# Optimization experiments

Hardware: AMD Instinct MI355X
Metric: run time of the kernel (lower is better)

## Reference

```python
import jax, jax.numpy as jnp
import numpy as np

BS, N, K, D = 8, 2048, 32, 64
H_MOD, H_STATE, H_MSG = 128, 128, 128
NB, BSZ, NG, BPG = 4, 8, 1, 4  # dendritic tree: K = NB*BSZ, NB = NG*BPG
MOD_IN = K + 2 * D + 1   # 161
MOD_OUT = K + 1 + D      # 97
STATE_IN = 2 * D + 1     # 129
MSG_IN = 2 * D           # 128


def setup_inputs() -> dict:
    key = jax.random.key(0)
    ks = jax.random.split(key, 16)

    def w(k, shape, fan_sum):
        return jax.random.normal(k, shape, jnp.float32) * (2.0 / fan_sum) ** 0.5

    inp = {
        'h': jax.random.normal(ks[0], (BS, N, D), jnp.float32) * 0.1,
        'prev_messages': jax.random.normal(ks[1], (BS, N, D), jnp.float32) * 0.1,
        'hebbian_traces': jax.random.uniform(ks[2], (BS, N, K), jnp.float32),
        'decay_logit': jax.random.normal(ks[3], (BS, N), jnp.float32),
        'primitives': jax.random.normal(ks[4], (BS, N, D), jnp.float32) * 0.1,
        'mod_w1': w(ks[5], (N, H_MOD, MOD_IN), MOD_IN + H_MOD),
        'mod_b1': jnp.zeros((N, H_MOD), jnp.float32),
        'mod_w2': w(ks[6], (N, H_MOD, MOD_OUT), H_MOD + MOD_OUT),
        'mod_b2': jnp.zeros((N, MOD_OUT), jnp.float32),
        'state_w1': w(ks[7], (N, H_STATE, STATE_IN), STATE_IN + H_STATE),
        'state_b1': jnp.zeros((N, H_STATE), jnp.float32),
        'state_w2': w(ks[8], (N, H_STATE, D), H_STATE + D),
        'state_b2': jnp.zeros((N, D), jnp.float32),
        'msg_w1': w(ks[9], (N, H_MSG, MSG_IN), MSG_IN + H_MSG),
        'msg_b1': jnp.zeros((N, H_MSG), jnp.float32),
        'msg_w2': w(ks[10], (N, H_MSG, D), H_MSG + D),
        'msg_b2': jnp.zeros((N, D), jnp.float32),
        'dendrite_branch_w': jnp.full((N, NB, BSZ, D), 1.0 / BSZ, jnp.float32),
        'dendrite_group_w': jnp.full((N, NG, BPG, D), 1.0 / BPG, jnp.float32),
        'conn_indices': jnp.sort(jax.random.randint(ks[11], (N, K), 0, N), axis=-1),
    }
    return inp


def reference(h, prev_messages, hebbian_traces, decay_logit, primitives,
              mod_w1, mod_b1, mod_w2, mod_b2,
              state_w1, state_b1, state_w2, state_b2,
              msg_w1, msg_b1, msg_w2, msg_b2,
              dendrite_branch_w, dendrite_group_w, conn_indices):
    # --- segment-boundary modulator: per-neuron 2-layer MLP ---
    mod_in = jnp.concatenate(
        [hebbian_traces, h, decay_logit[..., None], primitives], axis=-1)  # [B,N,MOD_IN]
    hid = jnp.tanh(jnp.einsum('bni,nhi->bnh', mod_in, mod_w1) + mod_b1)
    mod_out = jnp.einsum('bnh,nho->bno', hid, mod_w2) + mod_b2  # [B,N,MOD_OUT]
    new_w_conn = mod_out[..., :K]          # [B,N,K]
    new_decay_logit = mod_out[..., K]      # [B,N]
    new_primitives = mod_out[..., K + 1:]  # [B,N,D]

    # --- gather + weight + dendritic tree reduction ---
    w_sig = jax.nn.sigmoid(new_w_conn)                 # [B,N,K]
    neighbor_msgs = prev_messages[:, conn_indices]     # [B,N,K,D]
    weighted = w_sig[..., None] * neighbor_msgs        # [B,N,K,D]
    tree = weighted.reshape(BS, N, NB, BSZ, D)
    branch_out = jnp.tanh((tree * dendrite_branch_w[None]).sum(axis=3))   # [B,N,NB,D]
    grouped = branch_out.reshape(BS, N, NG, BPG, D)
    group_out = jnp.tanh((grouped * dendrite_group_w[None]).sum(axis=3))  # [B,N,NG,D]
    received = group_out.mean(axis=2)                  # [B,N,D]  (n_tree == K: no leftover)

    # --- per-neuron state MLP ---
    decay = jax.nn.sigmoid(new_decay_logit)
    sx = jnp.concatenate([received, h, decay[..., None]], axis=-1)  # [B,N,STATE_IN]
    sh = jnp.tanh(jnp.einsum('bni,nhi->bnh', sx, state_w1) + state_b1)
    h_new = jnp.tanh(jnp.einsum('bnh,nhd->bnd', sh, state_w2) + state_b2)  # [B,N,D]

    # --- per-neuron message MLP ---
    mx = jnp.concatenate([h_new, new_primitives], axis=-1)  # [B,N,MSG_IN]
    mh = jnp.tanh(jnp.einsum('bni,nhi->bnh', mx, msg_w1) + msg_b1)
    msg = jnp.tanh(jnp.einsum('bnh,nhd->bnd', mh, msg_w2) + msg_b2)  # [B,N,D]

    return jnp.stack([h_new, msg])  # [2,B,N,D]
```

## Files before the change

kernel.cpp:

```cpp
#include <hip/hip_runtime.h>
#include <stdint.h>

#define BSZB 256

constexpr int BB = 8;
constexpr int NN = 2048;
constexpr int KK = 32;
constexpr int DD = 64;
constexpr int HH = 128;
constexpr int SIN = 164;

__device__ __forceinline__ float sigmoidf_(float x) { return 1.0f / (1.0f + expf(-x)); }

template<int L, int WSTRIDE>
__device__ __forceinline__ void gemmA(const float* __restrict__ Wg,
                                      const float* __restrict__ bias,
                                      const float* s_in, float* s_w, float* s_hid,
                                      int t)
{
    const int hl = t & 31;
    const int b  = t >> 5;
    #pragma unroll 1
    for (int tile = 0; tile < 4; ++tile) {
        const float* wt = Wg + tile * 32 * L;
        if constexpr (WSTRIDE == L) {
            constexpr int nvec = (32 * L) / 4;
            for (int v = t; v < nvec; v += BSZB)
                *(float4*)(s_w + v * 4) = *(const float4*)(wt + v * 4);
        } else {
            constexpr int elems = 32 * L;
            #pragma unroll
            for (int it = 0; it < elems / (BSZB * 4); ++it) {
                int e = t * 4 + it * (BSZB * 4);
                float4 v = *(const float4*)(wt + e);
                int hr = e >> 7, c = e & 127;
                float* dst = s_w + hr * WSTRIDE + c;
                dst[0] = v.x; dst[1] = v.y; dst[2] = v.z; dst[3] = v.w;
            }
        }
        __syncthreads();
        const float* wr = s_w + hl * WSTRIDE;
        const float* ir = s_in + b * SIN;
        float a0 = 0.f, a1 = 0.f, a2 = 0.f, a3 = 0.f;
        constexpr int L4 = L & ~3;
        #pragma unroll 4
        for (int i = 0; i < L4; i += 4) {
            float4 iv = *(const float4*)(ir + i);
            a0 += wr[i+0] * iv.x;
            a1 += wr[i+1] * iv.y;
            a2 += wr[i+2] * iv.z;
            a3 += wr[i+3] * iv.w;
        }
        if constexpr (L4 < L) {
            #pragma unroll
            for (int i = L4; i < L; ++i) a0 += wr[i] * ir[i];
        }
        float acc = (a0 + a1) + (a2 + a3);
        int hg = tile * 32 + hl;
        s_hid[b * HH + hg] = tanhf(acc + bias[hg]);
        __syncthreads();
    }
}

__global__ __launch_bounds__(BSZB, 4) void memgraph_kernel(
    const float* __restrict__ g_h,   const float* __restrict__ g_pm,
    const float* __restrict__ g_heb, const float* __restrict__ g_dlog,
    const float* __restrict__ g_prim,
    const float* __restrict__ mw1, const float* __restrict__ mb1,
    const float* __restrict__ mw2, const float* __restrict__ mb2,
    const float* __restrict__ sw1, const float* __restrict__ sb1,
    const float* __restrict__ sw2, const float* __restrict__ sb2,
    const float* __restrict__ xw1, const float* __restrict__ xb1,
    const float* __restrict__ xw2, const float* __restrict__ xb2,
    const float* __restrict__ dbw, const float* __restrict__ dgw,
    const int* __restrict__ conn, float* __restrict__ out)
{
    const int n = blockIdx.x;
    const int t = threadIdx.x;

    __shared__ float s_w[32 * 161];
    __shared__ float s_in[BB * SIN];
    __shared__ float s_hid[BB * HH];
    __shared__ float s_hc[BB * DD];
    __shared__ float s_wsig[BB * KK];
    __shared__ float s_np[BB * DD];
    __shared__ float s_dec[BB];
    __shared__ float s_recv[BB * DD];
    __shared__ float s_hnew[BB * DD];
    __shared__ int   s_conn[KK];

    {
        int b = t >> 5, k = t & 31;
        s_in[b * SIN + k] = g_heb[(b * NN + n) * KK + k];
        #pragma unroll
        for (int r = 0; r < 2; ++r) {
            int e = t + r * BSZB, bb = e >> 6, d = e & 63;
            float hv = g_h[(bb * NN + n) * DD + d];
            s_in[bb * SIN + 32 + d] = hv;
            s_hc[bb * DD + d] = hv;
            s_in[bb * SIN + 97 + d] = g_prim[(bb * NN + n) * DD + d];
        }
        if (t < BB) s_in[t * SIN + 96] = g_dlog[t * NN + n];
        if (t < KK) s_conn[t] = conn[n * KK + t];
    }
    __syncthreads();

    gemmA<161, 161>(mw1 + (size_t)n * HH * 161, mb1 + n * HH, s_in, s_w, s_hid, t);

    {
        const float* w2 = mw2 + (size_t)n * HH * 97;
        int o = t & 127, bg = t >> 7;
        if (o < 97) {
            const float* hs = s_hid + (bg * 4) * HH;
            float a[4] = {0.f, 0.f, 0.f, 0.f};
            #pragma unroll 4
            for (int hq = 0; hq < HH / 4; ++hq) {
                float wv[4];
                #pragma unroll
                for (int j = 0; j < 4; ++j) wv[j] = w2[(hq * 4 + j) * 97 + o];
                #pragma unroll
                for (int bb2 = 0; bb2 < 4; ++bb2) {
                    float hv[4];
                    *(float4*)hv = *(const float4*)(hs + bb2 * HH + hq * 4);
                    #pragma unroll
                    for (int j = 0; j < 4; ++j) a[bb2] += hv[j] * wv[j];
                }
            }
            float bv = mb2[n * 97 + o];
            #pragma unroll
            for (int j = 0; j < 4; ++j) {
                int b = bg * 4 + j; float v = a[j] + bv;
                if (o < KK)        s_wsig[b * KK + o] = sigmoidf_(v);
                else if (o == KK)  s_dec[b] = sigmoidf_(v);
                else               s_np[b * DD + o - KK - 1] = v;
            }
        }
    }
    __syncthreads();

    {
        int d = t & 63;
        #pragma unroll 1
        for (int pass = 0; pass < 2; ++pass) {
            int b = pass * 4 + (t >> 6);
            float gsum = 0.f;
            #pragma unroll
            for (int br = 0; br < 4; ++br) {
                float acc = 0.f;
                #pragma unroll
                for (int s = 0; s < 8; ++s) {
                    int ci = s_conn[br * 8 + s];
                    float m = g_pm[((size_t)b * NN + ci) * DD + d];
                    acc += m * s_wsig[b * KK + br * 8 + s]
                             * dbw[(size_t)n * 2048 + (br * 8 + s) * DD + d];
                }
                gsum += tanhf(acc) * dgw[(size_t)n * 256 + br * DD + d];
            }
            s_recv[b * DD + d] = tanhf(gsum);
        }
    }
    __syncthreads();

    {
        #pragma unroll
        for (int r = 0; r < 2; ++r) {
            int e = t + r * BSZB, b = e >> 6, d = e & 63;
            s_in[b * SIN + d]      = s_recv[b * DD + d];
            s_in[b * SIN + 64 + d] = s_hc[b * DD + d];
        }
        if (t < BB) s_in[t * SIN + 128] = s_dec[t];
    }
    __syncthreads();

    gemmA<129, 129>(sw1 + (size_t)n * HH * 129, sb1 + n * HH, s_in, s_w, s_hid, t);

    {
        const float* w = sw2 + (size_t)n * HH * DD;
        int d = t & 63, bg = t >> 6;
        const float* h0 = s_hid + (bg * 2 + 0) * HH;
        const float* h1 = s_hid + (bg * 2 + 1) * HH;
        float a0 = 0.f, a1 = 0.f;
        #pragma unroll 4
        for (int hq = 0; hq < HH / 4; ++hq) {
            float hv0[4], hv1[4];
            *(float4*)hv0 = *(const float4*)(h0 + hq * 4);
            *(float4*)hv1 = *(const float4*)(h1 + hq * 4);
            #pragma unroll
            for (int j = 0; j < 4; ++j) {
                float wv = w[(hq * 4 + j) * DD + d];
                a0 += hv0[j] * wv; a1 += hv1[j] * wv;
            }
        }
        float bv = sb2[n * DD + d];
        float v0 = tanhf(a0 + bv), v1 = tanhf(a1 + bv);
        s_hnew[(bg * 2 + 0) * DD + d] = v0;
        s_hnew[(bg * 2 + 1) * DD + d] = v1;
        out[((size_t)(bg * 2 + 0) * NN + n) * DD + d] = v0;
        out[((size_t)(bg * 2 + 1) * NN + n) * DD + d] = v1;
    }
    __syncthreads();

    {
        #pragma unroll
        for (int r = 0; r < 2; ++r) {
            int e = t + r * BSZB, b = e >> 6, d = e & 63;
            s_in[b * SIN + d]      = s_hnew[b * DD + d];
            s_in[b * SIN + 64 + d] = s_np[b * DD + d];
        }
    }
    __syncthreads();

    gemmA<128, 129>(xw1 + (size_t)n * HH * 128, xb1 + n * HH, s_in, s_w, s_hid, t);

    {
        const float* w = xw2 + (size_t)n * HH * DD;
        int d = t & 63, bg = t >> 6;
        const float* h0 = s_hid + (bg * 2 + 0) * HH;
        const float* h1 = s_hid + (bg * 2 + 1) * HH;
        float a0 = 0.f, a1 = 0.f;
        #pragma unroll 4
        for (int hq = 0; hq < HH / 4; ++hq) {
            float hv0[4], hv1[4];
            *(float4*)hv0 = *(const float4*)(h0 + hq * 4);
            *(float4*)hv1 = *(const float4*)(h1 + hq * 4);
            #pragma unroll
            for (int j = 0; j < 4; ++j) {
                float wv = w[(hq * 4 + j) * DD + d];
                a0 += hv0[j] * wv; a1 += hv1[j] * wv;
            }
        }
        float bv = xb2[n * DD + d];
        size_t base = (size_t)BB * NN * DD;
        out[base + ((size_t)(bg * 2 + 0) * NN + n) * DD + d] = tanhf(a0 + bv);
        out[base + ((size_t)(bg * 2 + 1) * NN + n) * DD + d] = tanhf(a1 + bv);
    }
}

extern "C" void kernel_launch(void* const* d_in, const int* in_sizes, int n_in,
                              void* d_out, int out_size, void* d_ws, size_t ws_size,
                              hipStream_t stream) {
    memgraph_kernel<<<dim3(NN), dim3(BSZB), 0, stream>>>(
        (const float*)d_in[0],  (const float*)d_in[1],  (const float*)d_in[2],
        (const float*)d_in[3],  (const float*)d_in[4],  (const float*)d_in[5],
        (const float*)d_in[6],  (const float*)d_in[7],  (const float*)d_in[8],
        (const float*)d_in[9],  (const float*)d_in[10], (const float*)d_in[11],
        (const float*)d_in[12], (const float*)d_in[13], (const float*)d_in[14],
        (const float*)d_in[15], (const float*)d_in[16], (const float*)d_in[17],
        (const float*)d_in[18], (const int*)d_in[19],   (float*)d_out);
}
```

Baseline: 652.4 us.

## Register-prefetch next weight tile and split gemmA reduction across threads

The first-layer GEMM helper now loads the next 32-row weight tile into registers while the current tile is being computed, then writes it to shared memory after the barrier. This overlaps global loads with compute instead of stalling on them. Each thread also now handles a slice of the input dimension for all 8 batch rows, so every weight value read from shared memory is reused 8 times. Partial sums go to a new shared buffer and are reduced in a second phase. The change adds register pressure and shared memory, so the occupancy hint is lowered from 4 to 3 blocks.

```diff
diff --git a/kernel.cpp b/kernel.cpp
--- a/kernel.cpp
+++ b/kernel.cpp
@@ -15,54 +15,90 @@
 template<int L, int WSTRIDE>
 __device__ __forceinline__ void gemmA(const float* __restrict__ Wg,
                                       const float* __restrict__ bias,
-                                      const float* s_in, float* s_w, float* s_hid,
-                                      int t)
+                                      const float* s_in, float* s_w, float* s_part,
+                                      float* s_hid, int t)
 {
     const int hl = t & 31;
-    const int b  = t >> 5;
+    const int kc = t >> 5;
+    constexpr int NV  = 8 * L;
+    constexpr int PRE = (NV + BSZB - 1) / BSZB;
+    constexpr int NJ  = L / 32;
+    constexpr int I0  = 32 * NJ;
+
+    float4 pre[PRE];
+    {
+        int c = 0;
+        for (int v = t; v < NV; v += BSZB) pre[c++] = *(const float4*)(Wg + 4 * v);
+        c = 0;
+        for (int v = t; v < NV; v += BSZB) {
+            if constexpr (WSTRIDE == L) {
+                *(float4*)(s_w + 4 * v) = pre[c++];
+            } else {
+                int e = 4 * v; int hr = e >> 7; int cc = e & 127;
+                float4 q = pre[c++];
+                float* dd = s_w + hr * WSTRIDE + cc;
+                dd[0] = q.x; dd[1] = q.y; dd[2] = q.z; dd[3] = q.w;
+            }
+        }
+    }
+    __syncthreads();
+
     #pragma unroll 1
     for (int tile = 0; tile < 4; ++tile) {
-        const float* wt = Wg + tile * 32 * L;
-        if constexpr (WSTRIDE == L) {
-            constexpr int nvec = (32 * L) / 4;
-            for (int v = t; v < nvec; v += BSZB)
-                *(float4*)(s_w + v * 4) = *(const float4*)(wt + v * 4);
-        } else {
-            constexpr int elems = 32 * L;
-            #pragma unroll
-            for (int it = 0; it < elems / (BSZB * 4); ++it) {
-                int e = t * 4 + it * (BSZB * 4);
-                float4 v = *(const float4*)(wt + e);
-                int hr = e >> 7, c = e & 127;
-                float* dst = s_w + hr * WSTRIDE + c;
-                dst[0] = v.x; dst[1] = v.y; dst[2] = v.z; dst[3] = v.w;
-            }
-        }
+        if (tile < 3) {
+            const float* wn = Wg + (tile + 1) * 32 * L;
+            int c = 0;
+            for (int v = t; v < NV; v += BSZB) pre[c++] = *(const float4*)(wn + 4 * v);
+        }
+        float acc[BB] = {0.f, 0.f, 0.f, 0.f, 0.f, 0.f, 0.f, 0.f};
+        const float* wr = s_w + hl * WSTRIDE;
+        #pragma unroll
+        for (int j = 0; j < NJ; ++j) {
+            int i = 4 * (kc + 8 * j);
+            float w0 = wr[i + 0], w1 = wr[i + 1], w2_ = wr[i + 2], w3 = wr[i + 3];
+            #pragma unroll
+            for (int b = 0; b < BB; ++b) {
+                float4 iv = *(const float4*)(s_in + b * SIN + i);
+                acc[b] += w0 * iv.x + w1 * iv.y + w2_ * iv.z + w3 * iv.w;
+            }
+        }
+        if constexpr (I0 < L) {
+            if (kc == 0) {
+                float wv = wr[I0];
+                #pragma unroll
+                for (int b = 0; b < BB; ++b) acc[b] += wv * s_in[b * SIN + I0];
+            }
+        }
+        #pragma unroll
+        for (int b = 0; b < BB; ++b) s_part[kc * 256 + b * 32 + hl] = acc[b];
         __syncthreads();
-        const float* wr = s_w + hl * WSTRIDE;
-        const float* ir = s_in + b * SIN;
-        float a0 = 0.f, a1 = 0.f, a2 = 0.f, a3 = 0.f;
-        constexpr int L4 = L & ~3;
-        #pragma unroll 4
-        for (int i = 0; i < L4; i += 4) {
-            float4 iv = *(const float4*)(ir + i);
-            a0 += wr[i+0] * iv.x;
-            a1 += wr[i+1] * iv.y;
-            a2 += wr[i+2] * iv.z;
-            a3 += wr[i+3] * iv.w;
-        }
-        if constexpr (L4 < L) {
-            #pragma unroll
-            for (int i = L4; i < L; ++i) a0 += wr[i] * ir[i];
-        }
-        float acc = (a0 + a1) + (a2 + a3);
-        int hg = tile * 32 + hl;
-        s_hid[b * HH + hg] = tanhf(acc + bias[hg]);
+
+        if (tile < 3) {
+            int c = 0;
+            for (int v = t; v < NV; v += BSZB) {
+                if constexpr (WSTRIDE == L) {
+                    *(float4*)(s_w + 4 * v) = pre[c++];
+                } else {
+                    int e = 4 * v; int hr = e >> 7; int cc = e & 127;
+                    float4 q = pre[c++];
+                    float* dd = s_w + hr * WSTRIDE + cc;
+                    dd[0] = q.x; dd[1] = q.y; dd[2] = q.z; dd[3] = q.w;
+                }
+            }
+        }
+        {
+            int hl2 = t & 31, b2 = t >> 5;
+            float s = 0.f;
+            #pragma unroll
+            for (int k2 = 0; k2 < 8; ++k2) s += s_part[k2 * 256 + b2 * 32 + hl2];
+            int hg = tile * 32 + hl2;
+            s_hid[b2 * HH + hg] = tanhf(s + bias[hg]);
+        }
         __syncthreads();
     }
 }
 
-__global__ __launch_bounds__(BSZB, 4) void memgraph_kernel(
+__global__ __launch_bounds__(BSZB, 3) void memgraph_kernel(
     const float* __restrict__ g_h,   const float* __restrict__ g_pm,
     const float* __restrict__ g_heb, const float* __restrict__ g_dlog,
     const float* __restrict__ g_prim,
@@ -79,6 +115,7 @@
     const int t = threadIdx.x;
 
     __shared__ float s_w[32 * 161];
+    __shared__ float s_part[8 * BB * 32];
     __shared__ float s_in[BB * SIN];
     __shared__ float s_hid[BB * HH];
     __shared__ float s_hc[BB * DD];
@@ -105,7 +142,7 @@
     }
     __syncthreads();
 
-    gemmA<161, 161>(mw1 + (size_t)n * HH * 161, mb1 + n * HH, s_in, s_w, s_hid, t);
+    gemmA<161, 161>(mw1 + (size_t)n * HH * 161, mb1 + n * HH, s_in, s_w, s_part, s_hid, t);
 
     {
         const float* w2 = mw2 + (size_t)n * HH * 97;
@@ -172,7 +209,7 @@
     }
     __syncthreads();
 
-    gemmA<129, 129>(sw1 + (size_t)n * HH * 129, sb1 + n * HH, s_in, s_w, s_hid, t);
+    gemmA<129, 129>(sw1 + (size_t)n * HH * 129, sb1 + n * HH, s_in, s_w, s_part, s_hid, t);
 
     {
         const float* w = sw2 + (size_t)n * HH * DD;
@@ -210,7 +247,7 @@
     }
     __syncthreads();
 
-    gemmA<128, 129>(xw1 + (size_t)n * HH * 128, xb1 + n * HH, s_in, s_w, s_hid, t);
+    gemmA<128, 129>(xw1 + (size_t)n * HH * 128, xb1 + n * HH, s_in, s_w, s_part, s_hid, t);
 
     {
         const float* w = xw2 + (size_t)n * HH * DD;
```

New measurement: 787.3 us. 1.21x slower.
